# Kernel tuning notes

Hardware: AMD Instinct MI355X
Metric: run time of the kernel (lower is better)

Reference implementation:

```python
import jax, jax.numpy as jnp
import numpy as np

B, S, E, H, D = 4, 2048, 1024, 16, 64


def setup_inputs() -> dict:
    key = jax.random.key(0)
    ks = jax.random.split(key, 6)
    scale_in = 1.0 / np.sqrt(E)
    return {
        "x": jax.random.normal(ks[0], (B, S, E), dtype=jnp.float32),
        "Wq": jax.random.normal(ks[1], (H, E, D), dtype=jnp.float32) * scale_in,
        "bq": jnp.zeros((H, D), dtype=jnp.float32),
        "Wk": jax.random.normal(ks[2], (H, E, D), dtype=jnp.float32) * scale_in,
        "bk": jnp.zeros((H, D), dtype=jnp.float32),
        "Wv": jax.random.normal(ks[3], (H, E, D), dtype=jnp.float32) * scale_in,
        "bv": jnp.zeros((H, D), dtype=jnp.float32),
        "Wo": jax.random.normal(ks[4], (H * D, E), dtype=jnp.float32) * (1.0 / np.sqrt(H * D)),
        "bo": jnp.zeros((E,), dtype=jnp.float32),
    }


def reference(x, Wq, bq, Wk, bk, Wv, bv, Wo, bo):
    # Per-head Q/K/V projections, batched over heads: [B,S,E] x [H,E,D] -> [B,H,S,D]
    q = jnp.einsum("bse,hed->bhsd", x, Wq) + bq[None, :, None, :]
    k = jnp.einsum("bse,hed->bhsd", x, Wk) + bk[None, :, None, :]
    v = jnp.einsum("bse,hed->bhsd", x, Wv) + bv[None, :, None, :]

    d = q.shape[-1]
    scores = jnp.einsum("bhqd,bhkd->bhqk", q, k) / jnp.sqrt(jnp.asarray(d, q.dtype))
    # Causal mask (registered tril buffer of size max_seq_len in HeadAttention)
    seq = scores.shape[-1]
    causal = jnp.tril(jnp.ones((seq, seq), dtype=bool))
    scores = jnp.where(causal[None, None, :, :], scores, jnp.asarray(-1e9, scores.dtype))
    attn = jax.nn.softmax(scores, axis=-1)
    out = jnp.einsum("bhqk,bhkd->bhqd", attn, v)  # [B,H,S,D]

    # Concat heads: [B,S,H*D], then output projection (dropout is identity in eval)
    out = out.transpose(0, 2, 1, 3).reshape(out.shape[0], out.shape[2], -1)
    return out @ Wo + bo
```

## Files before the change

kernel.cpp:

```cpp
#include <hip/hip_runtime.h>

typedef __bf16 bf16x8 __attribute__((ext_vector_type(8)));
typedef __bf16 bf16x4 __attribute__((ext_vector_type(4)));
typedef float  f32x4  __attribute__((ext_vector_type(4)));

#define B_    4
#define S_    2048
#define E_    1024
#define H_    16
#define D_    64
#define MROWS (B_*S_)

#define SCORE_SCALE 0.18033688011112043f

__device__ __forceinline__ void load_lds16(const void* g, void* l) {
  __builtin_amdgcn_global_load_lds((__attribute__((address_space(1))) void*)g,
                                   (__attribute__((address_space(3))) void*)l,
                                   16, 0, 0);
}

__device__ __forceinline__ f32x4 mfma16(bf16x8 a, bf16x8 b, f32x4 c) {
  return __builtin_amdgcn_mfma_f32_16x16x32_bf16(a, b, c, 0, 0, 0);
}

__device__ __forceinline__ int swz(int row, int dchunk) {
  return row * 64 + ((dchunk ^ (row & 7)) * 8);
}


__global__ void prep(const float4* __restrict__ x, const float* __restrict__ Wq,
                     const float* __restrict__ Wk, const float* __restrict__ Wv,
                     const float* __restrict__ bq, const float* __restrict__ bk,
                     const float* __restrict__ bv, const float* __restrict__ Wo,
                     __bf16* __restrict__ xb, __bf16* __restrict__ Wt,
                     float* __restrict__ bqkv, __bf16* __restrict__ Wot) {
  __shared__ float t[64][65];
  int bid = blockIdx.x;
  if (bid < 8192) {
    int id = bid * 256 + threadIdx.x;
    float4 v = x[id];
    bf16x4 o = { (__bf16)v.x, (__bf16)v.y, (__bf16)v.z, (__bf16)v.w };
    *(bf16x4*)(xb + 4 * (size_t)id) = o;
    return;
  }
  int tx = threadIdx.x & 63;
  int ty = threadIdx.x >> 6;
  if (bid < 8960) {
    int b2 = bid - 8192;
    int e0 = (b2 & 15) * 64;
    int h  = (b2 >> 4) & 15;
    int p  = b2 >> 8;
    const float* W    = (p == 0) ? Wq : (p == 1) ? Wk : Wv;
    const float* bsrc = (p == 0) ? bq : (p == 1) ? bk : bv;
#pragma unroll
    for (int r = 0; r < 16; ++r) {
      int eL = ty + r * 4;
      t[eL][tx] = W[((size_t)h * 1024 + (e0 + eL)) * 64 + tx];
    }
    __syncthreads();
#pragma unroll
    for (int r = 0; r < 16; ++r) {
      int d = ty + r * 4;
      Wt[((size_t)(p * 1024 + h * 64 + d)) * 1024 + e0 + tx] = (__bf16)t[tx][d];
    }
    if ((b2 & 15) == 0 && threadIdx.x < 64)
      bqkv[p * 1024 + h * 64 + threadIdx.x] = bsrc[h * 64 + threadIdx.x];
  } else {
    int b2 = bid - 8960;
    int hd0 = (b2 >> 4) * 64;
    int e0  = (b2 & 15) * 64;
#pragma unroll
    for (int r = 0; r < 16; ++r) {
      int hdL = ty + r * 4;
      t[hdL][tx] = Wo[(size_t)(hd0 + hdL) * 1024 + e0 + tx];
    }
    __syncthreads();
#pragma unroll
    for (int r = 0; r < 16; ++r) {
      int eL = ty + r * 4;
      Wot[(size_t)(e0 + eL) * 1024 + hd0 + tx] = (__bf16)t[tx][eL];
    }
  }
}


template <int MODE, int BN, int NDIM>
__global__ __launch_bounds__(512, 1) void gemm8p(const __bf16* __restrict__ A,
                                                 const __bf16* __restrict__ Bt,
                                                 const float* __restrict__ bias,
                                                 void* __restrict__ Cout,
                                                 __bf16* __restrict__ VT) {
  constexpr int K = 1024;
  constexpr int NB = BN / 64;
  constexpr int WC = BN / 4;
  __shared__ __attribute__((aligned(16))) __bf16 As[2 * 256 * 64];
  __shared__ __attribute__((aligned(16))) __bf16 Bs[2 * BN * 64];

  int tid = threadIdx.x, wave = tid >> 6, lane = tid & 63;
  int quad = lane >> 4, cc = lane & 15;
  constexpr int nb = NDIM / BN;
  int nwg = (int)gridDim.x;
  int bid = (int)blockIdx.x;
  bid = (bid & 7) * (nwg >> 3) + (bid >> 3);
  int bm = bid / nb, bn = bid % nb;
  const __bf16* Abase = A + (size_t)bm * 256 * K;
  const __bf16* Bbase = Bt + (size_t)bn * BN * K;
  int wrow = (wave >> 2) * 128;
  int wcol = (wave & 3) * WC;

  f32x4 acc[8][NB];
#pragma unroll
  for (int m = 0; m < 8; ++m)
#pragma unroll
    for (int n = 0; n < NB; ++n) acc[m][n] = (f32x4){0.f, 0.f, 0.f, 0.f};

  int srl = tid >> 3;
  int sch = tid & 7;
  int scol = (sch ^ (srl & 7)) * 8;

#define STAGE_A(t, sub, buf)                                                   \
  load_lds16(Abase + (size_t)((sub) * 64 + srl) * K + (t) * 64 + scol,         \
             &As[(buf) * 16384 + (sub) * 4096 + tid * 8])
#define STAGE_B(t, sub, buf)                                                   \
  load_lds16(Bbase + (size_t)((sub) * 64 + srl) * K + (t) * 64 + scol,         \
             &Bs[(buf) * (BN * 64) + (sub) * 4096 + tid * 8])

#pragma unroll
  for (int s = 0; s < 4; ++s) STAGE_A(0, s, 0);
#pragma unroll
  for (int s = 0; s < NB; ++s) STAGE_B(0, s, 0);
#pragma unroll
  for (int s = 0; s < 4; ++s) STAGE_A(1, s, 1);
  asm volatile("s_waitcnt vmcnt(4)" ::: "memory");
  __builtin_amdgcn_sched_barrier(0);
  asm volatile("s_barrier" ::: "memory");

  bf16x8 af[8][2], bfr[NB][2];

#define RD_B(buf)                                                              \
  _Pragma("unroll") for (int n = 0; n < NB; ++n)                               \
      _Pragma("unroll") for (int kk = 0; kk < 2; ++kk)                         \
          bfr[n][kk] = *(const bf16x8*)&Bs[(buf) * (BN * 64) +                 \
                                           swz(wcol + n * 16 + cc, kk * 4 + quad)]
#define RD_A(buf, mlo)                                                         \
  _Pragma("unroll") for (int m = mlo; m < (mlo) + 4; ++m)                      \
      _Pragma("unroll") for (int kk = 0; kk < 2; ++kk)                         \
          af[m][kk] = *(const bf16x8*)&As[(buf) * 16384 +                      \
                                          swz(wrow + m * 16 + cc, kk * 4 + quad)]
#define MFMA_PAIR(q)                                                           \
  do {                                                                         \
    __builtin_amdgcn_s_setprio(1);                                             \
    _Pragma("unroll") for (int m2 = 0; m2 < 2; ++m2)                           \
        _Pragma("unroll") for (int n = 0; n < NB; ++n)                         \
            _Pragma("unroll") for (int kk = 0; kk < 2; ++kk)                   \
                acc[(q) * 2 + m2][n] =                                         \
                    mfma16(af[(q) * 2 + m2][kk], bfr[n][kk],                   \
                           acc[(q) * 2 + m2][n]);                              \
    __builtin_amdgcn_s_setprio(0);                                             \
  } while (0)
#define LGKM0                                                                  \
  asm volatile("s_waitcnt lgkmcnt(0)" ::: "memory");                           \
  __builtin_amdgcn_sched_barrier(0)
#define BAR asm volatile("s_barrier" ::: "memory")

#pragma unroll 1
  for (int it = 0; it < 8; ++it) {
    int b_t = 2 * it + 1;
    int c_t = (2 * it + 2) & 15;
    int d_t = (2 * it + 3) & 15;
    RD_B(0); RD_A(0, 0);
    STAGE_B(b_t, 0, 1); STAGE_B(b_t, 1, 1);
    LGKM0; MFMA_PAIR(0); BAR;
    RD_A(0, 4);
    if (NB >= 3) STAGE_B(b_t, 2, 1);
    if (NB >= 4) STAGE_B(b_t, 3, 1);
    LGKM0; MFMA_PAIR(1); BAR;
    STAGE_A(c_t, 0, 0); STAGE_A(c_t, 1, 0);
    MFMA_PAIR(2); BAR;
    STAGE_A(c_t, 2, 0); STAGE_A(c_t, 3, 0);
    MFMA_PAIR(3);
    asm volatile("s_waitcnt vmcnt(4)" ::: "memory");
    __builtin_amdgcn_sched_barrier(0);
    BAR;
    RD_B(1); RD_A(1, 0);
    STAGE_B(c_t, 0, 0); STAGE_B(c_t, 1, 0);
    LGKM0; MFMA_PAIR(0); BAR;
    RD_A(1, 4);
    if (NB >= 3) STAGE_B(c_t, 2, 0);
    if (NB >= 4) STAGE_B(c_t, 3, 0);
    LGKM0; MFMA_PAIR(1); BAR;
    STAGE_A(d_t, 0, 1); STAGE_A(d_t, 1, 1);
    MFMA_PAIR(2); BAR;
    STAGE_A(d_t, 2, 1); STAGE_A(d_t, 3, 1);
    MFMA_PAIR(3);
    asm volatile("s_waitcnt vmcnt(4)" ::: "memory");
    __builtin_amdgcn_sched_barrier(0);
    BAR;
  }
  asm volatile("s_waitcnt vmcnt(0)" ::: "memory");

#pragma unroll
  for (int n = 0; n < NB; ++n) {
    int gcol = bn * BN + wcol + n * 16 + cc;
    float bv = bias[gcol];
#pragma unroll
    for (int m = 0; m < 8; ++m) {
      int grow0 = bm * 256 + wrow + m * 16 + quad * 4;
      if (MODE == 0) {
#pragma unroll
        for (int r = 0; r < 4; ++r)
          ((float*)Cout)[(size_t)(grow0 + r) * NDIM + gcol] = acc[m][n][r] + bv;
      } else if (gcol < 2048) {
        float sc = (gcol < 1024) ? SCORE_SCALE : 1.0f;
#pragma unroll
        for (int r = 0; r < 4; ++r)
          ((__bf16*)Cout)[(size_t)(grow0 + r) * 2048 + gcol] =
              (__bf16)((acc[m][n][r] + bv) * sc);
      } else {
        int bh = (grow0 >> 11) * 16 + ((gcol >> 6) & 15);
        int d  = gcol & 63;
        bf16x4 pk;
#pragma unroll
        for (int r = 0; r < 4; ++r) pk[r] = (__bf16)(acc[m][n][r] + bv);
        *(bf16x4*)&VT[((size_t)(bh * 64 + d)) * 2048 + (grow0 & 2047)] = pk;
      }
    }
  }
#undef STAGE_A
#undef STAGE_B
#undef RD_B
#undef RD_A
#undef MFMA_PAIR
#undef LGKM0
#undef BAR
}


__global__ __launch_bounds__(256, 3) void attn(const __bf16* __restrict__ QKb,
                                               const __bf16* __restrict__ VT,
                                               __bf16* __restrict__ O) {
  int bx = blockIdx.x;
  int bh = bx & 63;
  int g  = bx >> 6;
  int qt = (g < 8) ? (15 - g) : (g - 8);
  int h  = bh & 15;
  int b  = bh >> 4;
  int q0 = qt * 128;
  int tid = threadIdx.x, wave = tid >> 6, lane = tid & 63;
  int quad = lane >> 4, c = lane & 15;

  __shared__ __attribute__((aligned(16))) __bf16 smem[24576];
  __bf16* Qs = smem;
  __bf16* Ks = smem + 8192;
  __bf16* Vs = smem + 16384;
  __bf16* Ps = smem + wave * 2048;

  const __bf16* Qbase = QKb + (size_t)(b * S_ + q0) * 2048 + h * 64;
  const __bf16* Vbase = VT + (size_t)bh * (64 * 2048);
#pragma unroll
  for (int p = 0; p < 4; ++p) {
    int gi = tid + p * 256;
    int row = gi >> 3, pch = gi & 7;
    load_lds16(Qbase + (size_t)row * 2048 + (pch ^ (row & 7)) * 8, &Qs[gi * 8]);
  }
  {
    const __bf16* Kb = QKb + (size_t)(b * S_) * 2048 + 1024 + h * 64;
#pragma unroll
    for (int p = 0; p < 2; ++p) {
      int gi = tid + p * 256;
      int row = gi >> 3, pch = gi & 7;
      load_lds16(Kb + (size_t)row * 2048 + (pch ^ (row & 7)) * 8, &Ks[gi * 8]);
      load_lds16(Vbase + (size_t)row * 2048 + (pch ^ (row & 7)) * 8, &Vs[gi * 8]);
    }
  }
  __syncthreads();

  bf16x8 qf[2][2];
#pragma unroll
  for (int i = 0; i < 2; ++i)
#pragma unroll
    for (int kk = 0; kk < 2; ++kk)
      qf[i][kk] = *(const bf16x8*)&Qs[swz(wave * 32 + i * 16 + c, kk * 4 + quad)];

  const __bf16 one_b = (__bf16)1.0f;
  bf16x8 ones = { one_b, one_b, one_b, one_b, one_b, one_b, one_b, one_b };

  f32x4 acc_o[2][4], acc_l[2];
#pragma unroll
  for (int i = 0; i < 2; ++i) {
    acc_l[i] = (f32x4){0.f, 0.f, 0.f, 0.f};
#pragma unroll
    for (int j = 0; j < 4; ++j) acc_o[i][j] = (f32x4){0.f, 0.f, 0.f, 0.f};
  }

  int qwave = q0 + wave * 32;
  int ntiles = qt * 2 + 2;
  for (int t = 0; t < ntiles; ++t) {
    int cur = t & 1;
    if (t + 1 < ntiles) {
      int kv1 = (t + 1) * 64;
      const __bf16* Kb = QKb + (size_t)(b * S_ + kv1) * 2048 + 1024 + h * 64;
      const __bf16* Vb = Vbase + kv1;
#pragma unroll
      for (int p = 0; p < 2; ++p) {
        int gi = tid + p * 256;
        int row = gi >> 3, pch = gi & 7;
        load_lds16(Kb + (size_t)row * 2048 + (pch ^ (row & 7)) * 8,
                   &Ks[(cur ^ 1) * 4096 + gi * 8]);
        load_lds16(Vb + (size_t)row * 2048 + (pch ^ (row & 7)) * 8,
                   &Vs[(cur ^ 1) * 4096 + gi * 8]);
      }
    }

    int kv0 = t * 64;
    if (kv0 <= qwave + 31) {
      const __bf16* Kc = Ks + cur * 4096;
      const __bf16* Vc = Vs + cur * 4096;

      f32x4 acc_t[2][4];
#pragma unroll
      for (int i = 0; i < 2; ++i)
#pragma unroll
        for (int j = 0; j < 4; ++j) acc_t[i][j] = (f32x4){0.f, 0.f, 0.f, 0.f};
      bf16x8 kf[4][2];
#pragma unroll
      for (int j = 0; j < 4; ++j)
#pragma unroll
        for (int kk = 0; kk < 2; ++kk)
          kf[j][kk] = *(const bf16x8*)&Kc[swz(j * 16 + c, kk * 4 + quad)];
      __builtin_amdgcn_s_setprio(1);
#pragma unroll
      for (int i = 0; i < 2; ++i)
#pragma unroll
        for (int j = 0; j < 4; ++j)
#pragma unroll
          for (int kk = 0; kk < 2; ++kk)
            acc_t[i][j] = mfma16(kf[j][kk], qf[i][kk], acc_t[i][j]);
      __builtin_amdgcn_s_setprio(0);

      bool domask = (kv0 + 63 > qwave);
#pragma unroll
      for (int i = 0; i < 2; ++i) {
        int q_l = i * 16 + c;
        int q_g = qwave + q_l;
#pragma unroll
        for (int j = 0; j < 4; ++j) {
          bf16x4 pk;
#pragma unroll
          for (int r = 0; r < 4; ++r) {
            float p = __builtin_amdgcn_exp2f(acc_t[i][j][r]);
            if (domask) {
              int kv = kv0 + j * 16 + quad * 4 + r;
              p = (kv > q_g) ? 0.f : p;
            }
            pk[r] = (__bf16)p;
          }
          int dch8 = j * 2 + (quad >> 1);
          int phys = q_l * 64 + ((dch8 ^ (q_l & 7)) * 8) + (quad & 1) * 4;
          *(bf16x4*)&Ps[phys] = pk;
        }
      }

      bf16x8 pf[2][2], vf[4][2];
#pragma unroll
      for (int i = 0; i < 2; ++i)
#pragma unroll
        for (int kk = 0; kk < 2; ++kk)
          pf[i][kk] = *(const bf16x8*)&Ps[swz(i * 16 + c, kk * 4 + quad)];
#pragma unroll
      for (int j = 0; j < 4; ++j)
#pragma unroll
        for (int kk = 0; kk < 2; ++kk)
          vf[j][kk] = *(const bf16x8*)&Vc[swz(j * 16 + c, kk * 4 + quad)];
      __builtin_amdgcn_s_setprio(1);
#pragma unroll
      for (int i = 0; i < 2; ++i) {
#pragma unroll
        for (int j = 0; j < 4; ++j)
#pragma unroll
          for (int kk = 0; kk < 2; ++kk)
            acc_o[i][j] = mfma16(pf[i][kk], vf[j][kk], acc_o[i][j]);
        acc_l[i] = mfma16(pf[i][0], ones, acc_l[i]);
        acc_l[i] = mfma16(pf[i][1], ones, acc_l[i]);
      }
      __builtin_amdgcn_s_setprio(0);
    }

    __syncthreads();
  }

  __bf16* Obase = O + (size_t)(b * S_ + q0) * 1024 + h * 64;
#pragma unroll
  for (int i = 0; i < 2; ++i)
#pragma unroll
    for (int r = 0; r < 4; ++r) {
      float rl = 1.0f / acc_l[i][r];
      int row = wave * 32 + i * 16 + quad * 4 + r;
#pragma unroll
      for (int j = 0; j < 4; ++j)
        Obase[(size_t)row * 1024 + j * 16 + c] = (__bf16)(acc_o[i][j][r] * rl);
    }
}


extern "C" void kernel_launch(void* const* d_in, const int* in_sizes, int n_in,
                              void* d_out, int out_size, void* d_ws, size_t ws_size,
                              hipStream_t stream) {
  (void)in_sizes; (void)n_in; (void)out_size; (void)ws_size;
  const float* x  = (const float*)d_in[0];
  const float* Wq = (const float*)d_in[1];
  const float* bq = (const float*)d_in[2];
  const float* Wk = (const float*)d_in[3];
  const float* bk = (const float*)d_in[4];
  const float* Wv = (const float*)d_in[5];
  const float* bv = (const float*)d_in[6];
  const float* Wo = (const float*)d_in[7];
  const float* bo = (const float*)d_in[8];

  char* w = (char*)d_ws;
  __bf16* xb   = (__bf16*)(w);
  __bf16* Wt   = (__bf16*)(w + (16ull << 20));
  __bf16* Wot  = (__bf16*)(w + (22ull << 20));
  float*  bqkv = (float*) (w + (24ull << 20));
  __bf16* QKb  = (__bf16*)(w + (25ull << 20));
  __bf16* Ob   = (__bf16*)(w + (57ull << 20));
  __bf16* VT   = (__bf16*)(w + (73ull << 20));

  prep<<<9216, 256, 0, stream>>>((const float4*)x, Wq, Wk, Wv, bq, bk, bv, Wo,
                                 xb, Wt, bqkv, Wot);
  gemm8p<1, 256, 3072><<<384, 512, 0, stream>>>(xb, Wt, bqkv, (void*)QKb, VT);
  attn<<<1024, 256, 0, stream>>>(QKb, VT, Ob);
  gemm8p<0, 128, 1024><<<256, 512, 0, stream>>>(Ob, Wot, bo, d_out, nullptr);
}
```

Baseline: 258.6 us.

## Add dedicated QKV GEMM kernel with interleaved LDS staging and MFMA schedule

Adds a specialised 256x256-tile QKV projection kernel. It interleaves global-to-LDS staging of the next A/B tiles with quarter-tile MFMA blocks, using explicit waitcnt, barriers and setprio so loads overlap compute. It replaces the generic templated gemm for the QKV stage. The output projection gemm's launch bounds also change to allow two workgroups per CU, which may raise register pressure or cause spills.

```diff
diff --git a/kernel.cpp b/kernel.cpp
--- a/kernel.cpp
+++ b/kernel.cpp
@@ -84,8 +84,152 @@
 }
 
 
+__global__ __launch_bounds__(512, 1) void gemm8q(const __bf16* __restrict__ A,
+                                                 const __bf16* __restrict__ Bt,
+                                                 const float* __restrict__ bias,
+                                                 __bf16* __restrict__ QKb,
+                                                 __bf16* __restrict__ VT) {
+  constexpr int K = 1024;
+  __shared__ __attribute__((aligned(16))) __bf16 As[2 * 256 * 64];
+  __shared__ __attribute__((aligned(16))) __bf16 Bs[2 * 256 * 64];
+
+  int tid = threadIdx.x, wave = tid >> 6, lane = tid & 63;
+  int quad = lane >> 4, cc = lane & 15;
+  int nwg = (int)gridDim.x;
+  int bid = (int)blockIdx.x;
+  bid = (bid & 7) * (nwg >> 3) + (bid >> 3);
+  int bm = bid / 12, bn = bid % 12;
+  const __bf16* Abase = A + (size_t)bm * 256 * K;
+  const __bf16* Bbase = Bt + (size_t)bn * 256 * K;
+  int wrow = (wave >> 2) * 128;
+  int wcol = (wave & 3) * 64;
+
+  f32x4 acc[8][4];
+#pragma unroll
+  for (int m = 0; m < 8; ++m)
+#pragma unroll
+    for (int n = 0; n < 4; ++n) acc[m][n] = (f32x4){0.f, 0.f, 0.f, 0.f};
+
+  int srl = tid >> 3;
+  int sch = tid & 7;
+  int scol = (sch ^ (srl & 7)) * 8;
+
+#define STAGE_A(t, sub, buf)                                                   \
+  load_lds16(Abase + (size_t)((sub) * 64 + srl) * K + (t) * 64 + scol,         \
+             &As[(buf) * 16384 + (sub) * 4096 + tid * 8])
+#define STAGE_B(t, sub, buf)                                                   \
+  load_lds16(Bbase + (size_t)((sub) * 64 + srl) * K + (t) * 64 + scol,         \
+             &Bs[(buf) * 16384 + (sub) * 4096 + tid * 8])
+
+#pragma unroll
+  for (int s = 0; s < 4; ++s) STAGE_A(0, s, 0);
+#pragma unroll
+  for (int s = 0; s < 4; ++s) STAGE_B(0, s, 0);
+#pragma unroll
+  for (int s = 0; s < 4; ++s) STAGE_B(1, s, 1);
+  asm volatile("s_waitcnt vmcnt(4)" ::: "memory");
+  __builtin_amdgcn_sched_barrier(0);
+  asm volatile("s_barrier" ::: "memory");
+
+  bf16x8 af[4][2], bfr[4][2];
+
+#define RD_A4(buf, half)                                                       \
+  _Pragma("unroll") for (int m2 = 0; m2 < 4; ++m2)                             \
+      _Pragma("unroll") for (int kk = 0; kk < 2; ++kk)                         \
+          af[m2][kk] = *(const bf16x8*)&As[(buf) * 16384 +                     \
+              swz(wrow + ((half) * 4 + m2) * 16 + cc, kk * 4 + quad)]
+#define RD_B2(buf, npair)                                                      \
+  _Pragma("unroll") for (int n2 = 0; n2 < 2; ++n2)                             \
+      _Pragma("unroll") for (int kk = 0; kk < 2; ++kk)                         \
+          bfr[(npair) * 2 + n2][kk] = *(const bf16x8*)&Bs[(buf) * 16384 +      \
+              swz(wcol + ((npair) * 2 + n2) * 16 + cc, kk * 4 + quad)]
+#define MFMA_Q(mlo, npair)                                                     \
+  do {                                                                         \
+    __builtin_amdgcn_s_setprio(1);                                             \
+    _Pragma("unroll") for (int m2 = 0; m2 < 4; ++m2)                           \
+        _Pragma("unroll") for (int n2 = 0; n2 < 2; ++n2)                       \
+            _Pragma("unroll") for (int kk = 0; kk < 2; ++kk)                   \
+                acc[(mlo) + m2][(npair) * 2 + n2] =                            \
+                    mfma16(af[m2][kk], bfr[(npair) * 2 + n2][kk],              \
+                           acc[(mlo) + m2][(npair) * 2 + n2]);                 \
+    __builtin_amdgcn_s_setprio(0);                                             \
+  } while (0)
+#define LGKM0                                                                  \
+  asm volatile("s_waitcnt lgkmcnt(0)" ::: "memory");                           \
+  __builtin_amdgcn_sched_barrier(0)
+#define VMC4                                                                   \
+  asm volatile("s_waitcnt vmcnt(4)" ::: "memory");                             \
+  __builtin_amdgcn_sched_barrier(0)
+#define BAR asm volatile("s_barrier" ::: "memory")
+
+#pragma unroll 1
+  for (int it = 0; it < 8; ++it) {
+    int b_t = 2 * it + 1;
+    int c_t = (2 * it + 2) & 15;
+    int d_t = (2 * it + 3) & 15;
+    RD_A4(0, 0); RD_B2(0, 0);
+    STAGE_A(b_t, 0, 1); STAGE_A(b_t, 1, 1);
+    LGKM0; MFMA_Q(0, 0); BAR;
+    RD_B2(0, 1);
+    STAGE_A(b_t, 2, 1); STAGE_A(b_t, 3, 1);
+    LGKM0; MFMA_Q(0, 1); BAR;
+    RD_A4(0, 1);
+    STAGE_B(c_t, 0, 0); STAGE_B(c_t, 1, 0);
+    LGKM0; MFMA_Q(4, 0); BAR;
+    STAGE_B(c_t, 2, 0); STAGE_B(c_t, 3, 0);
+    MFMA_Q(4, 1);
+    VMC4; BAR;
+    RD_A4(1, 0); RD_B2(1, 0);
+    STAGE_A(c_t, 0, 0); STAGE_A(c_t, 1, 0);
+    LGKM0; MFMA_Q(0, 0); BAR;
+    RD_B2(1, 1);
+    STAGE_A(c_t, 2, 0); STAGE_A(c_t, 3, 0);
+    LGKM0; MFMA_Q(0, 1); BAR;
+    RD_A4(1, 1);
+    STAGE_B(d_t, 0, 1); STAGE_B(d_t, 1, 1);
+    LGKM0; MFMA_Q(4, 0); BAR;
+    STAGE_B(d_t, 2, 1); STAGE_B(d_t, 3, 1);
+    MFMA_Q(4, 1);
+    VMC4; BAR;
+  }
+  asm volatile("s_waitcnt vmcnt(0)" ::: "memory");
+
+#pragma unroll
+  for (int n = 0; n < 4; ++n) {
+    int gcol = bn * 256 + wcol + n * 16 + cc;
+    float bv = bias[gcol];
+#pragma unroll
+    for (int m = 0; m < 8; ++m) {
+      int grow0 = bm * 256 + wrow + m * 16 + quad * 4;
+      if (gcol < 2048) {
+        float sc = (gcol < 1024) ? SCORE_SCALE : 1.0f;
+#pragma unroll
+        for (int r = 0; r < 4; ++r)
+          QKb[(size_t)(grow0 + r) * 2048 + gcol] =
+              (__bf16)((acc[m][n][r] + bv) * sc);
+      } else {
+        int bh = (grow0 >> 11) * 16 + ((gcol >> 6) & 15);
+        int d  = gcol & 63;
+        bf16x4 pk;
+#pragma unroll
+        for (int r = 0; r < 4; ++r) pk[r] = (__bf16)(acc[m][n][r] + bv);
+        *(bf16x4*)&VT[((size_t)(bh * 64 + d)) * 2048 + (grow0 & 2047)] = pk;
+      }
+    }
+  }
+#undef STAGE_A
+#undef STAGE_B
+#undef RD_A4
+#undef RD_B2
+#undef MFMA_Q
+#undef LGKM0
+#undef VMC4
+#undef BAR
+}
+
+
 template <int MODE, int BN, int NDIM>
-__global__ __launch_bounds__(512, 1) void gemm8p(const __bf16* __restrict__ A,
+__global__ __launch_bounds__(512, 2) void gemm8p(const __bf16* __restrict__ A,
                                                  const __bf16* __restrict__ Bt,
                                                  const float* __restrict__ bias,
                                                  void* __restrict__ Cout,
@@ -428,7 +572,7 @@
 
   prep<<<9216, 256, 0, stream>>>((const float4*)x, Wq, Wk, Wv, bq, bk, bv, Wo,
                                  xb, Wt, bqkv, Wot);
-  gemm8p<1, 256, 3072><<<384, 512, 0, stream>>>(xb, Wt, bqkv, (void*)QKb, VT);
+  gemm8q<<<384, 512, 0, stream>>>(xb, Wt, bqkv, QKb, VT);
   attn<<<1024, 256, 0, stream>>>(QKb, VT, Ob);
   gemm8p<0, 128, 1024><<<256, 512, 0, stream>>>(Ob, Wot, bo, d_out, nullptr);
 }
```

After: 252.6 us. -2.3%, faster.
